# Kernel optimization log

Measured on AMD Instinct MI355X. Metric: run time of the kernel, lower is better.

## Reference

```python
import jax, jax.numpy as jnp
import numpy as np

TAU = 2.0
V_TH = 1.0
PI = float(np.pi)
T = 3

@jax.custom_vjp
def spike(x):
    # Heaviside spike; backward uses ATan surrogate (alpha=2.0) as in spikingjelly
    return (x >= 0.0).astype(x.dtype)

def _spike_fwd(x):
    return spike(x), x

def _spike_bwd(x, g):
    # d/dx of (1/pi) atan(pi/2 * alpha * x) + 1/2 with alpha=2 => 1/(1+(pi*x)^2)
    return (g / (1.0 + (PI * x) ** 2),)

spike.defvjp(_spike_fwd, _spike_bwd)

def lif_step(v, x):
    # decay_input=True, v_reset=0.0 hard reset: v += (x - v)/tau
    v = v + (x - v) / TAU
    s = spike(v - V_TH)
    v = v * (1.0 - s)
    return v, s

def setup_inputs() -> dict:
    key = jax.random.key(0)
    ks = jax.random.split(key, 7)
    B, D, H, O = 16384, 2752, 256, 100
    dvs = jax.random.normal(ks[0], (B, T, D), dtype=jnp.float32)
    W1 = jax.random.normal(ks[1], (H, D), dtype=jnp.float32) * (1.0 / np.sqrt(D))
    b1 = jnp.zeros((H,), dtype=jnp.float32)
    W2 = jax.random.normal(ks[2], (H, H), dtype=jnp.float32) * (1.0 / np.sqrt(H))
    b2 = jnp.zeros((H,), dtype=jnp.float32)
    W3 = jax.random.normal(ks[3], (O, H), dtype=jnp.float32) * (1.0 / np.sqrt(H))
    b3 = jnp.zeros((O,), dtype=jnp.float32)
    return {"dvs": dvs, "W1": W1, "b1": b1, "W2": W2, "b2": b2, "W3": W3, "b3": b3}

def reference(dvs, W1, b1, W2, b2, W3, b3):
    # dvs: [B, T, D] -> [T, B, D]
    x_tbd = jnp.swapaxes(dvs, 0, 1)
    B = dvs.shape[0]
    v1 = jnp.zeros((B, W1.shape[0]), dtype=dvs.dtype)
    v2 = jnp.zeros((B, W2.shape[0]), dtype=dvs.dtype)
    v3 = jnp.zeros((B, W3.shape[0]), dtype=dvs.dtype)
    out = None
    for t in range(T):  # fixed T=3, state carried across steps
        h = x_tbd[t] @ W1.T + b1
        v1, s1 = lif_step(v1, h)
        h = s1 @ W2.T + b2
        v2, s2 = lif_step(v2, h)
        h = s2 @ W3.T + b3
        v3, s3 = lif_step(v3, h)
        out = s3
    return out  # spikes at last timestep, [B, 100]
```

## Files before the change

### kernel.cpp

```cpp
#include <hip/hip_runtime.h>

#define B_SZ    16384
#define T_STEPS 3
#define D_IN    2752
#define H_SZ    256
#define O_SZ    100
#define LDA     (T_STEPS * D_IN)

typedef short bf16x8 __attribute__((ext_vector_type(8)));
typedef float f32x4  __attribute__((ext_vector_type(4)));

__device__ __forceinline__ unsigned short f2bf(float x) {
  union { float f; unsigned int u; } v; v.f = x;
  unsigned int r = v.u + 0x7FFFu + ((v.u >> 16) & 1u);
  return (unsigned short)(r >> 16);
}

__device__ __forceinline__ void gload_lds16(const void* g, void* l) {
  __builtin_amdgcn_global_load_lds(
      (const __attribute__((address_space(1))) unsigned int*)g,
      (__attribute__((address_space(3))) unsigned int*)l, 16, 0, 0);
}

__global__ void cvt_w1_kernel(const float* __restrict__ W1,
                              unsigned short* __restrict__ W1bf) {
  int i = (blockIdx.x * 256 + threadIdx.x) * 4;
  float4 v = *(const float4*)(W1 + i);
  unsigned short o[4] = {f2bf(v.x), f2bf(v.y), f2bf(v.z), f2bf(v.w)};
  *(uint2*)(W1bf + i) = *(uint2*)o;
}

#define BM 64
#define BN 256
#define BK 32
#define NT (D_IN / BK)
#define LDK 40

__device__ __forceinline__ void stage_B(const unsigned short* __restrict__ W1bf,
                                        unsigned short (*Bbuf)[BK],
                                        int k0, int tid) {
  const int lane = tid & 63, w = tid >> 6;
#pragma unroll
  for (int q = 0; q < 4; ++q) {
    int g = (w * 4 + q) * 64 + lane;
    int r = g >> 2, c = g & 3;
    int cp = c ^ ((r >> 1) & 3);
    const unsigned short* src = W1bf + (size_t)r * D_IN + k0 + cp * 8;
    gload_lds16(src, &Bbuf[(w * 4 + q) * 16][0]);
  }
}

__global__ __launch_bounds__(256, 3) void gemm1_mfma_kernel(
    const float* __restrict__ dvs, const unsigned short* __restrict__ W1bf,
    const float* __restrict__ b1, float* __restrict__ Hout) {
  __shared__ __attribute__((aligned(16))) unsigned short Ab[2][BM][LDK];
  __shared__ __attribute__((aligned(16))) unsigned short Bb[2][BN][BK];

  const int r0   = blockIdx.x * BM;
  const int t    = r0 >> 14;
  const int brow = r0 & (B_SZ - 1);
  const float* Abase = dvs + (size_t)brow * LDA + t * D_IN;

  const int tid  = threadIdx.x;
  const int lane = tid & 63, wv = tid >> 6;
  const int wn0  = wv * 64;
  const int lrow = lane & 15;
  const int kgrp = lane >> 4;
  const int pidx = kgrp ^ ((lrow >> 1) & 3);

  const int s_row = tid >> 2;
  const int s_kq  = (tid & 3) << 3;
  const float* ap0 = Abase + (size_t)s_row * LDA + s_kq;

  f32x4 acc[4][4] = {};

  {
    float4 a0 = *(const float4*)(ap0);
    float4 a1 = *(const float4*)(ap0 + 4);
    stage_B(W1bf, Bb[0], 0, tid);
    unsigned short a8[8] = {f2bf(a0.x), f2bf(a0.y), f2bf(a0.z), f2bf(a0.w),
                            f2bf(a1.x), f2bf(a1.y), f2bf(a1.z), f2bf(a1.w)};
    *(uint4*)&Ab[0][s_row][s_kq] = *(uint4*)a8;
  }
  __syncthreads();

  int cur = 0;
  for (int k = 0; k < NT; ++k) {
    const bool pf = (k + 1 < NT);
    float4 a0n, a1n;
    if (pf) {
      const int k0n = (k + 1) * BK;
      a0n = *(const float4*)(ap0 + k0n);
      a1n = *(const float4*)(ap0 + k0n + 4);
      stage_B(W1bf, Bb[cur ^ 1], k0n, tid);
    }

    {
      const unsigned short (*Ac)[LDK] = Ab[cur];
      const unsigned short (*Bc)[BK]  = Bb[cur];
      bf16x8 af[4], bfr[4];
#pragma unroll
      for (int m = 0; m < 4; m++)
        af[m] = *(const bf16x8*)&Ac[m * 16 + lrow][kgrp * 8];
#pragma unroll
      for (int n = 0; n < 4; n++)
        bfr[n] = *(const bf16x8*)&Bc[wn0 + n * 16 + lrow][pidx * 8];
#pragma unroll
      for (int m = 0; m < 4; m++)
#pragma unroll
        for (int n = 0; n < 4; n++)
          acc[m][n] = __builtin_amdgcn_mfma_f32_16x16x32_bf16(
              af[m], bfr[n], acc[m][n], 0, 0, 0);
    }

    if (pf) {
      unsigned short a8[8] = {f2bf(a0n.x), f2bf(a0n.y), f2bf(a0n.z), f2bf(a0n.w),
                              f2bf(a1n.x), f2bf(a1n.y), f2bf(a1n.z), f2bf(a1n.w)};
      *(uint4*)&Ab[cur ^ 1][s_row][s_kq] = *(uint4*)a8;
    }
    __syncthreads();
    cur ^= 1;
  }

#pragma unroll
  for (int m = 0; m < 4; m++) {
    int gm = r0 + m * 16 + kgrp * 4;
#pragma unroll
    for (int n = 0; n < 4; n++) {
      int gn = wn0 + n * 16 + lrow;
      float bias = b1[gn];
#pragma unroll
      for (int r = 0; r < 4; r++)
        Hout[(size_t)(gm + r) * H_SZ + gn] = acc[m][n][r] + bias;
    }
  }
}

__global__ void transpose_kernel(const float* __restrict__ in,
                                 float* __restrict__ out, int rows, int cols) {
  __shared__ float tile[32][33];
  int bc = blockIdx.x * 32, br = blockIdx.y * 32;
  int tx = threadIdx.x, ty = threadIdx.y;
  for (int j = 0; j < 32; j += 8) {
    int r = br + ty + j, c = bc + tx;
    if (r < rows && c < cols) tile[ty + j][tx] = in[(size_t)r * cols + c];
  }
  __syncthreads();
  for (int j = 0; j < 32; j += 8) {
    int c = bc + ty + j, r = br + tx;
    if (c < cols && r < rows) out[(size_t)c * rows + r] = tile[tx][ty + j];
  }
}

__global__ __launch_bounds__(256) void recurrent2_kernel(
    const float* __restrict__ H, const float* __restrict__ W2T,
    const float* __restrict__ b2, const float* __restrict__ W3T,
    const float* __restrict__ b3, float* __restrict__ out) {
  const int tid = threadIdx.x, lane = tid & 63, wv = tid >> 6;
  const int b0 = blockIdx.x * 8 + wv * 2;

  float b2v[4];
#pragma unroll
  for (int q = 0; q < 4; q++) b2v[q] = b2[lane + 64 * q];
  const float b3a = b3[lane];
  const float b3b = (lane < O_SZ - 64) ? b3[64 + lane] : 0.f;

  for (int bi = 0; bi < 2; bi++) {
    const int b = b0 + bi;
    float v1[4] = {0.f, 0.f, 0.f, 0.f};
    float v2[4] = {0.f, 0.f, 0.f, 0.f};
    float v3a = 0.f, v3b = 0.f, s3a = 0.f, s3b = 0.f;

    for (int t = 0; t < T_STEPS; t++) {
      const float* hp = H + ((size_t)t * B_SZ + b) * H_SZ;
      unsigned long long m1[4];
      float h2[4] = {b2v[0], b2v[1], b2v[2], b2v[3]};
#pragma unroll
      for (int q = 0; q < 4; q++) {
        float h1 = hp[lane + 64 * q];
        v1[q] = 0.5f * (v1[q] + h1);
        bool s = (v1[q] >= 1.0f);
        m1[q] = __ballot(s);
        if (s) v1[q] = 0.f;
      }
#pragma unroll
      for (int q = 0; q < 4; q++) {
        unsigned long long m = m1[q];
        while (m) {
          int n = 64 * q + __builtin_ctzll(m);
          m &= m - 1;
          const float* wp = W2T + (size_t)n * H_SZ + lane;
          h2[0] += wp[0]; h2[1] += wp[64]; h2[2] += wp[128]; h2[3] += wp[192];
        }
      }
      unsigned long long m2[4];
#pragma unroll
      for (int q = 0; q < 4; q++) {
        v2[q] = 0.5f * (v2[q] + h2[q]);
        bool s = (v2[q] >= 1.0f);
        m2[q] = __ballot(s);
        if (s) v2[q] = 0.f;
      }
      float h3a = b3a, h3b = b3b;
#pragma unroll
      for (int q = 0; q < 4; q++) {
        unsigned long long m = m2[q];
        while (m) {
          int j = 64 * q + __builtin_ctzll(m);
          m &= m - 1;
          h3a += W3T[(size_t)j * O_SZ + lane];
          if (lane < O_SZ - 64) h3b += W3T[(size_t)j * O_SZ + 64 + lane];
        }
      }
      v3a = 0.5f * (v3a + h3a);
      v3b = 0.5f * (v3b + h3b);
      bool sa = (v3a >= 1.0f), sb = (v3b >= 1.0f);
      if (sa) v3a = 0.f;
      if (sb) v3b = 0.f;
      if (t == T_STEPS - 1) { s3a = sa ? 1.f : 0.f; s3b = sb ? 1.f : 0.f; }
    }
    out[(size_t)b * O_SZ + lane] = s3a;
    if (lane < O_SZ - 64) out[(size_t)b * O_SZ + 64 + lane] = s3b;
  }
}

extern "C" void kernel_launch(void* const* d_in, const int* in_sizes, int n_in,
                              void* d_out, int out_size, void* d_ws, size_t ws_size,
                              hipStream_t stream) {
  const float* dvs = (const float*)d_in[0];
  const float* W1  = (const float*)d_in[1];
  const float* b1  = (const float*)d_in[2];
  const float* W2  = (const float*)d_in[3];
  const float* b2  = (const float*)d_in[4];
  const float* W3  = (const float*)d_in[5];
  const float* b3  = (const float*)d_in[6];
  float* out = (float*)d_out;

  char* ws = (char*)d_ws;
  float* Hbuf = (float*)ws;
  float* W2T  = (float*)(ws + (size_t)T_STEPS * B_SZ * H_SZ * 4);
  float* W3T  = W2T + H_SZ * H_SZ;
  unsigned short* W1bf = (unsigned short*)(W3T + H_SZ * O_SZ);

  dim3 tb(32, 8);
  hipLaunchKernelGGL(cvt_w1_kernel, dim3((H_SZ * D_IN) / 1024), dim3(256),
                     0, stream, W1, W1bf);
  hipLaunchKernelGGL(transpose_kernel, dim3(8, 8), tb, 0, stream, W2, W2T, H_SZ, H_SZ);
  hipLaunchKernelGGL(transpose_kernel, dim3(8, 4), tb, 0, stream, W3, W3T, O_SZ, H_SZ);
  hipLaunchKernelGGL(gemm1_mfma_kernel, dim3((T_STEPS * B_SZ) / BM), dim3(256),
                     0, stream, dvs, W1bf, b1, Hbuf);
  hipLaunchKernelGGL(recurrent2_kernel, dim3(B_SZ / 8), dim3(256), 0, stream,
                     Hbuf, W2T, b2, W3T, b3, out);
}
```

Before: 835.5 us.

## Deepen GEMM1 prefetch with two-ahead A registers and manual waitcnt scheduling

Restructures the GEMM1 main loop into a 2x-unrolled ping-pong that keeps the fp32 A tile loads two K-steps ahead in registers. It replaces the generic __syncthreads with an explicit s_waitcnt vmcnt(2) plus s_barrier, fenced by sched_barriers, so the newest A global loads can stay in flight across the barrier. The aim is to hide more global-load latency behind the MFMA work. The cost is extra register pressure and hand-tuned wait counts that depend on how many loads each phase issues.

After: 828.5 us. No clear change (-0.8%).

```diff
diff --git a/kernel.cpp b/kernel.cpp
--- a/kernel.cpp
+++ b/kernel.cpp
@@ -50,6 +50,31 @@
   }
 }
 
+__device__ __forceinline__ void writeA(unsigned short (*dst)[LDK], int s_row,
+                                       int s_kq, float4 x, float4 y) {
+  unsigned short a8[8] = {f2bf(x.x), f2bf(x.y), f2bf(x.z), f2bf(x.w),
+                          f2bf(y.x), f2bf(y.y), f2bf(y.z), f2bf(y.w)};
+  *(uint4*)&dst[s_row][s_kq] = *(uint4*)a8;
+}
+
+__device__ __forceinline__ void mfma_phase(
+    const unsigned short (*Ac)[LDK], const unsigned short (*Bc)[BK],
+    f32x4 (&acc)[4][4], int lrow, int kgrp, int wn0, int pidx) {
+  bf16x8 af[4], bfr[4];
+#pragma unroll
+  for (int m = 0; m < 4; m++)
+    af[m] = *(const bf16x8*)&Ac[m * 16 + lrow][kgrp * 8];
+#pragma unroll
+  for (int n = 0; n < 4; n++)
+    bfr[n] = *(const bf16x8*)&Bc[wn0 + n * 16 + lrow][pidx * 8];
+#pragma unroll
+  for (int m = 0; m < 4; m++)
+#pragma unroll
+    for (int n = 0; n < 4; n++)
+      acc[m][n] = __builtin_amdgcn_mfma_f32_16x16x32_bf16(
+          af[m], bfr[n], acc[m][n], 0, 0, 0);
+}
+
 __global__ __launch_bounds__(256, 3) void gemm1_mfma_kernel(
     const float* __restrict__ dvs, const unsigned short* __restrict__ W1bf,
     const float* __restrict__ b1, float* __restrict__ Hout) {
@@ -74,53 +99,46 @@
 
   f32x4 acc[4][4] = {};
 
-  {
-    float4 a0 = *(const float4*)(ap0);
-    float4 a1 = *(const float4*)(ap0 + 4);
-    stage_B(W1bf, Bb[0], 0, tid);
-    unsigned short a8[8] = {f2bf(a0.x), f2bf(a0.y), f2bf(a0.z), f2bf(a0.w),
-                            f2bf(a1.x), f2bf(a1.y), f2bf(a1.z), f2bf(a1.w)};
-    *(uint4*)&Ab[0][s_row][s_kq] = *(uint4*)a8;
-  }
+  stage_B(W1bf, Bb[0], 0, tid);
+  float4 t0 = *(const float4*)(ap0);
+  float4 t1 = *(const float4*)(ap0 + 4);
+  float4 xA = *(const float4*)(ap0 + BK);
+  float4 yA = *(const float4*)(ap0 + BK + 4);
+  writeA(Ab[0], s_row, s_kq, t0, t1);
   __syncthreads();
-
-  int cur = 0;
-  for (int k = 0; k < NT; ++k) {
-    const bool pf = (k + 1 < NT);
-    float4 a0n, a1n;
-    if (pf) {
-      const int k0n = (k + 1) * BK;
-      a0n = *(const float4*)(ap0 + k0n);
-      a1n = *(const float4*)(ap0 + k0n + 4);
-      stage_B(W1bf, Bb[cur ^ 1], k0n, tid);
-    }
-
-    {
-      const unsigned short (*Ac)[LDK] = Ab[cur];
-      const unsigned short (*Bc)[BK]  = Bb[cur];
-      bf16x8 af[4], bfr[4];
-#pragma unroll
-      for (int m = 0; m < 4; m++)
-        af[m] = *(const bf16x8*)&Ac[m * 16 + lrow][kgrp * 8];
-#pragma unroll
-      for (int n = 0; n < 4; n++)
-        bfr[n] = *(const bf16x8*)&Bc[wn0 + n * 16 + lrow][pidx * 8];
-#pragma unroll
-      for (int m = 0; m < 4; m++)
-#pragma unroll
-        for (int n = 0; n < 4; n++)
-          acc[m][n] = __builtin_amdgcn_mfma_f32_16x16x32_bf16(
-              af[m], bfr[n], acc[m][n], 0, 0, 0);
-    }
-
-    if (pf) {
-      unsigned short a8[8] = {f2bf(a0n.x), f2bf(a0n.y), f2bf(a0n.z), f2bf(a0n.w),
-                              f2bf(a1n.x), f2bf(a1n.y), f2bf(a1n.z), f2bf(a1n.w)};
-      *(uint4*)&Ab[cur ^ 1][s_row][s_kq] = *(uint4*)a8;
-    }
-    __syncthreads();
-    cur ^= 1;
-  }
+  float4 xB, yB;
+
+  for (int k = 0; k < NT - 2; k += 2) {
+    stage_B(W1bf, Bb[1], (k + 1) * BK, tid);
+    __builtin_amdgcn_sched_barrier(0);
+    xB = *(const float4*)(ap0 + (k + 2) * BK);
+    yB = *(const float4*)(ap0 + (k + 2) * BK + 4);
+    __builtin_amdgcn_sched_barrier(0);
+    mfma_phase(Ab[0], Bb[0], acc, lrow, kgrp, wn0, pidx);
+    writeA(Ab[1], s_row, s_kq, xA, yA);
+    asm volatile("s_waitcnt vmcnt(2) lgkmcnt(0)" ::: "memory");
+    __builtin_amdgcn_sched_barrier(0);
+    __builtin_amdgcn_s_barrier();
+    __builtin_amdgcn_sched_barrier(0);
+
+    stage_B(W1bf, Bb[0], (k + 2) * BK, tid);
+    __builtin_amdgcn_sched_barrier(0);
+    xA = *(const float4*)(ap0 + (k + 3) * BK);
+    yA = *(const float4*)(ap0 + (k + 3) * BK + 4);
+    __builtin_amdgcn_sched_barrier(0);
+    mfma_phase(Ab[1], Bb[1], acc, lrow, kgrp, wn0, pidx);
+    writeA(Ab[0], s_row, s_kq, xB, yB);
+    asm volatile("s_waitcnt vmcnt(2) lgkmcnt(0)" ::: "memory");
+    __builtin_amdgcn_sched_barrier(0);
+    __builtin_amdgcn_s_barrier();
+    __builtin_amdgcn_sched_barrier(0);
+  }
+
+  stage_B(W1bf, Bb[1], (NT - 1) * BK, tid);
+  mfma_phase(Ab[0], Bb[0], acc, lrow, kgrp, wn0, pidx);
+  writeA(Ab[1], s_row, s_kq, xA, yA);
+  __syncthreads();
+  mfma_phase(Ab[1], Bb[1], acc, lrow, kgrp, wn0, pidx);
 
 #pragma unroll
   for (int m = 0; m < 4; m++) {
```
